# Kernel tuning notes

Measured on AMD Instinct MI355X. Metric: run time of the kernel, lower is better.

The kernel has to match this reference:

```python
import jax, jax.numpy as jnp
import numpy as np

N_NODES = 100000
N_EDGES = 1600000


def setup_inputs() -> dict:
    key = jax.random.key(0)
    k1, k2, k3, k4, k5, k6 = jax.random.split(key, 6)
    x = jax.random.normal(k1, (N_NODES, 2), dtype=jnp.float32)
    edge_index = jax.random.randint(k2, (2, N_EDGES), 0, N_NODES, dtype=jnp.int64)
    # Glorot-style init for GCN weights, zeros for biases (PyG defaults)
    W1 = jax.random.normal(k3, (2, 64), dtype=jnp.float32) * (1.0 / np.sqrt(2.0))
    b1 = jnp.zeros((64,), dtype=jnp.float32)
    W2 = jax.random.normal(k4, (64, 1), dtype=jnp.float32) * (1.0 / np.sqrt(64.0))
    b2 = jnp.zeros((1,), dtype=jnp.float32)
    return {"x": x, "edge_index": edge_index, "W1": W1, "b1": b1, "W2": W2, "b2": b2}


def reference(x, edge_index, W1, b1, W2, b2):
    N = x.shape[0]
    row, col = edge_index[0], edge_index[1]  # source, target (PyG flow source_to_target)
    # symmetric GCN normalization, degrees from target index (no self loops)
    deg = jax.ops.segment_sum(jnp.ones(edge_index.shape[1], x.dtype), col, num_segments=N)
    deg_inv_sqrt = jnp.where(deg > 0, jnp.where(deg > 0, deg, 1.0) ** -0.5, 0.0)
    norm = (deg_inv_sqrt[row] * deg_inv_sqrt[col])[:, None]  # [E,1]

    def gcn_conv(h, W, b):
        h = h @ W                       # [N,F_out] tiny GEMM
        msg = h[row] * norm             # gather + scale: [E,F_out]
        agg = jax.ops.segment_sum(msg, col, num_segments=N)  # scatter-add
        return agg + b

    h = jax.nn.relu(gcn_conv(x, W1, b1))   # dropout is identity in eval mode
    out = jax.nn.relu(gcn_conv(h, W2, b2))
    return out
```

## Files before the change

kernel.cpp:

```cpp
#include <hip/hip_runtime.h>
#include <math.h>

#define NN 100000
#define NE 1600000
#define BKT 448
#define NB 224
#define EPB 6400
#define NPB 250
#define STRIDE 8192
#define RT 1024

__global__ void __launch_bounds__(RT) reorder_kernel(
        const int* __restrict__ row, const int* __restrict__ col,
        unsigned* __restrict__ cursor, unsigned* __restrict__ packed) {
    __shared__ int h[NB], lb[NB];
    __shared__ unsigned gaddr[NB], glim[NB];
    __shared__ int wsum[RT / 64];
    __shared__ uint2 sga[EPB];
    const int t = threadIdx.x;
    const int lane = t & 63, wid = t >> 6;
    const int e0 = blockIdx.x * EPB;

    for (int i = t; i < NB; i += RT) h[i] = 0;
    __syncthreads();

    const int4* rv = (const int4*)(row + e0);
    const int4* cv = (const int4*)(col + e0);
    unsigned pk[8]; int bb[8];
#pragma unroll
    for (int u = 0; u < 8; ++u) bb[u] = -1;
#pragma unroll
    for (int g = 0; g < 2; ++g) {
        int grp = g * RT + t;
        if (grp < EPB / 4) {
            int4 r4 = rv[grp], c4 = cv[grp];
            int rr[4] = {r4.x, r4.y, r4.z, r4.w};
            int cc[4] = {c4.x, c4.y, c4.z, c4.w};
#pragma unroll
            for (int j = 0; j < 4; ++j) {
                int b = cc[j] / BKT;
                int cl = cc[j] - b * BKT;
                pk[4 * g + j] = ((unsigned)rr[j] << 9) | (unsigned)cl;
                bb[4 * g + j] = b;
            }
        }
    }
#pragma unroll
    for (int u = 0; u < 8; ++u)
        if (bb[u] >= 0) atomicAdd(&h[bb[u]], 1);
    __syncthreads();

    int v = (t < NB) ? h[t] : 0;
    int incl = v;
#pragma unroll
    for (int d = 1; d < 64; d <<= 1) {
        int u2 = __shfl_up(incl, d);
        if (lane >= d) incl += u2;
    }
    if (lane == 63) wsum[wid] = incl;
    __syncthreads();
    int off = 0;
#pragma unroll
    for (int j = 0; j < 3; ++j)
        if (j < wid) off += wsum[j];
    if (t < NB) {
        lb[t] = off + incl - v;
        unsigned base = v ? atomicAdd(&cursor[t], (unsigned)v) : 0u;
        gaddr[t] = (unsigned)t * STRIDE + base;
        glim[t]  = (unsigned)(t + 1) * STRIDE;
    }
    __syncthreads();
    for (int i = t; i < NB; i += RT) h[i] = 0;
    __syncthreads();

#pragma unroll
    for (int u = 0; u < 8; ++u) {
        if (bb[u] >= 0) {
            int b = bb[u];
            int r = atomicAdd(&h[b], 1);
            unsigned a = gaddr[b] + (unsigned)r;
            if (a >= glim[b]) a = 0xFFFFFFFFu;
            sga[lb[b] + r] = make_uint2(pk[u], a);
        }
    }
    __syncthreads();
    for (int i = t; i < EPB; i += RT) {
        uint2 e = sga[i];
        if (e.y != 0xFFFFFFFFu) packed[e.y] = e.x;
    }
}

__global__ void __launch_bounds__(RT) sortb_kernel(
        const unsigned* __restrict__ packed, const unsigned* __restrict__ cursor,
        const float2* __restrict__ x2,
        unsigned* __restrict__ srow, int2* __restrict__ node_rng,
        float* __restrict__ dis, float2* __restrict__ y2) {
    __shared__ int cnt[BKT], rk[BKT], sexA[BKT];
    __shared__ int wsum[(BKT + 63) / 64];
    __shared__ unsigned srt[STRIDE];
    const int t = threadIdx.x;
    const int lane = t & 63, wid = t >> 6;
    const int b = blockIdx.x;
    const unsigned s0 = (unsigned)b * STRIDE;
    const int L = min((int)cursor[b], STRIDE);
    const int L4 = L >> 2;

    for (int i = t; i < BKT; i += RT) { cnt[i] = 0; rk[i] = 0; }
    __syncthreads();

    const uint4* pv4 = (const uint4*)(packed + s0);
    for (int g = t; g < L4; g += RT) {
        uint4 p4 = pv4[g];
        atomicAdd(&cnt[p4.x & 511u], 1);
        atomicAdd(&cnt[p4.y & 511u], 1);
        atomicAdd(&cnt[p4.z & 511u], 1);
        atomicAdd(&cnt[p4.w & 511u], 1);
    }
    for (int i = 4 * L4 + t; i < L; i += RT)
        atomicAdd(&cnt[packed[s0 + i] & 511u], 1);
    __syncthreads();

    int v = (t < BKT) ? cnt[t] : 0;
    int incl = v;
#pragma unroll
    for (int d = 1; d < 64; d <<= 1) {
        int u2 = __shfl_up(incl, d);
        if (lane >= d) incl += u2;
    }
    if (lane == 63 && wid < (BKT + 63) / 64) wsum[wid] = incl;
    __syncthreads();
    int off = 0;
#pragma unroll
    for (int j = 0; j < (BKT + 63) / 64 - 1; ++j)
        if (j < wid) off += wsum[j];
    if (t < BKT) {
        int sex = off + incl - v;
        sexA[t] = sex;
        int node = b * BKT + t;
        if (node < NN) {
            float dv = (v > 0) ? rsqrtf((float)v) : 0.0f;
            dis[node] = dv;
            float2 xv = x2[node];
            y2[node] = make_float2(xv.x * dv, xv.y * dv);
            node_rng[node] = make_int2((int)(s0 + sex), (int)(s0 + sex + v));
        }
    }
    __syncthreads();

    for (int g = t; g < L4; g += RT) {
        uint4 p4 = pv4[g];
        unsigned pp[4] = {p4.x, p4.y, p4.z, p4.w};
#pragma unroll
        for (int j = 0; j < 4; ++j) {
            int cl = pp[j] & 511u;
            int r = atomicAdd(&rk[cl], 1);
            srt[sexA[cl] + r] = pp[j] >> 9;
        }
    }
    for (int i = 4 * L4 + t; i < L; i += RT) {
        unsigned p = packed[s0 + i];
        int cl = p & 511u;
        int r = atomicAdd(&rk[cl], 1);
        srt[sexA[cl] + r] = p >> 9;
    }
    __syncthreads();
    uint4* so4 = (uint4*)(srow + s0);
    for (int g = t; g < L4; g += RT) so4[g] = ((const uint4*)srt)[g];
    for (int i = 4 * L4 + t; i < L; i += RT) srow[s0 + i] = srt[i];
}

__global__ void conv1_kernel(const unsigned* __restrict__ srow, const int2* __restrict__ node_rng,
                             const float2* __restrict__ y2, const float* __restrict__ dis,
                             const float* __restrict__ W1, const float* __restrict__ b1,
                             const float* __restrict__ W2, float* __restrict__ z2) {
    __shared__ float sW0[64], sW1[64], sb1[64], sW2[64];
    int t = threadIdx.x;
    if (t < 64) { sW0[t] = W1[t]; sW1[t] = W1[64 + t]; sb1[t] = b1[t]; sW2[t] = W2[t]; }
    __syncthreads();
    int lane = t & 3;
    int node = blockIdx.x * 64 + (t >> 2);
    if (node >= NN) return;
    int2 rng = node_rng[node];
    float sx = 0.f, sy = 0.f;
    for (int k = rng.x + lane; k < rng.y; k += 4) {
        float2 v = y2[srow[k]];
        sx += v.x; sy += v.y;
    }
    sx += __shfl_xor(sx, 1); sy += __shfl_xor(sy, 1);
    sx += __shfl_xor(sx, 2); sy += __shfl_xor(sy, 2);
    float dv = dis[node];
    float a0 = sx * dv, a1 = sy * dv;
    float acc = 0.0f;
    int j0 = lane * 16;
#pragma unroll
    for (int jj = 0; jj < 16; ++jj) {
        int j = j0 + jj;
        float h = fmaf(a0, sW0[j], fmaf(a1, sW1[j], sb1[j]));
        acc = fmaf(fmaxf(h, 0.0f), sW2[j], acc);
    }
    acc += __shfl_xor(acc, 1);
    acc += __shfl_xor(acc, 2);
    if (lane == 0) z2[node] = acc * dv;
}

__global__ void conv2_kernel(const unsigned* __restrict__ srow, const int2* __restrict__ node_rng,
                             const float* __restrict__ z2, const float* __restrict__ dis,
                             const float* __restrict__ b2, float* __restrict__ out) {
    int t = threadIdx.x;
    int lane = t & 3;
    int node = blockIdx.x * 64 + (t >> 2);
    if (node >= NN) return;
    int2 rng = node_rng[node];
    float s = 0.f;
    for (int k = rng.x + lane; k < rng.y; k += 4)
        s += z2[srow[k]];
    s += __shfl_xor(s, 1);
    s += __shfl_xor(s, 2);
    if (lane == 0)
        out[node] = fmaxf(fmaf(dis[node], s, b2[0]), 0.0f);
}

extern "C" void kernel_launch(void* const* d_in, const int* in_sizes, int n_in,
                              void* d_out, int out_size, void* d_ws, size_t ws_size,
                              hipStream_t stream) {
    const float* x  = (const float*)d_in[0];
    const int*   ei = (const int*)d_in[1];
    const float* W1 = (const float*)d_in[2];
    const float* b1 = (const float*)d_in[3];
    const float* W2 = (const float*)d_in[4];
    const float* b2 = (const float*)d_in[5];
    float* out = (float*)d_out;

    const int* row = ei;
    const int* col = ei + NE;

    unsigned* packed   = (unsigned*)d_ws;
    unsigned* srow     = packed + (size_t)NB * STRIDE;
    float2*   y2       = (float2*)(srow + (size_t)NB * STRIDE);
    float*    dis      = (float*)(y2 + NN);
    float*    z2       = dis + NN;
    int2*     node_rng = (int2*)(z2 + NN);
    unsigned* cursor   = (unsigned*)(node_rng + NN);

    hipMemsetAsync(cursor, 0, NB * sizeof(unsigned), stream);

    reorder_kernel<<<NPB, RT, 0, stream>>>(row, col, cursor, packed);
    sortb_kernel  <<<NB, RT, 0, stream>>>(packed, cursor, (const float2*)x,
                                          srow, node_rng, dis, y2);
    conv1_kernel  <<<(NN + 63) / 64, 256, 0, stream>>>(srow, node_rng, y2, dis,
                                                       W1, b1, W2, z2);
    conv2_kernel  <<<(NN + 63) / 64, 256, 0, stream>>>(srow, node_rng, z2, dis, b2, out);
}
```

Measured before the change: 111.8 us.

## Split degree pass and fuse bucket sort with first GCN conv using LDS indices

Moves the degree/normalisation computation into its own kernel and fuses the per-bucket counting sort with the first convolution, so conv1 reads neighbour indices from shared memory instead of re-reading srow from global. Each node's segment is padded to a multiple of four, which enables uint4 index loads in both conv1 and conv2; STRIDE grows to make room for the padding. In exchange, the packed buffer is read one more time, conv1 now runs on only 224 blocks with fewer nodes processed in parallel, and the padding adds overflow clamping.

```diff
diff --git a/kernel.cpp b/kernel.cpp
--- a/kernel.cpp
+++ b/kernel.cpp
@@ -7,7 +7,7 @@
 #define NB 224
 #define EPB 6400
 #define NPB 250
-#define STRIDE 8192
+#define STRIDE 8960
 #define RT 1024
 
 __global__ void __launch_bounds__(RT) reorder_kernel(
@@ -90,22 +90,20 @@
     }
 }
 
-__global__ void __launch_bounds__(RT) sortb_kernel(
+__global__ void __launch_bounds__(RT) deg_kernel(
         const unsigned* __restrict__ packed, const unsigned* __restrict__ cursor,
-        const float2* __restrict__ x2,
-        unsigned* __restrict__ srow, int2* __restrict__ node_rng,
-        float* __restrict__ dis, float2* __restrict__ y2) {
-    __shared__ int cnt[BKT], rk[BKT], sexA[BKT];
-    __shared__ int wsum[(BKT + 63) / 64];
-    __shared__ unsigned srt[STRIDE];
+        const float2* __restrict__ x2, float* __restrict__ dis,
+        float2* __restrict__ y2, int2* __restrict__ node_rng) {
+    __shared__ int cnt[BKT];
+    __shared__ int wsum[7];
     const int t = threadIdx.x;
     const int lane = t & 63, wid = t >> 6;
     const int b = blockIdx.x;
-    const unsigned s0 = (unsigned)b * STRIDE;
+    const int s0 = b * STRIDE;
     const int L = min((int)cursor[b], STRIDE);
     const int L4 = L >> 2;
 
-    for (int i = t; i < BKT; i += RT) { cnt[i] = 0; rk[i] = 0; }
+    for (int i = t; i < BKT; i += RT) cnt[i] = 0;
     __syncthreads();
 
     const uint4* pv4 = (const uint4*)(packed + s0);
@@ -121,32 +119,66 @@
     __syncthreads();
 
     int v = (t < BKT) ? cnt[t] : 0;
-    int incl = v;
+    int vp = (v + 3) & ~3;
+    int incl = vp;
 #pragma unroll
     for (int d = 1; d < 64; d <<= 1) {
         int u2 = __shfl_up(incl, d);
         if (lane >= d) incl += u2;
     }
-    if (lane == 63 && wid < (BKT + 63) / 64) wsum[wid] = incl;
+    if (lane == 63 && wid < 7) wsum[wid] = incl;
     __syncthreads();
     int off = 0;
 #pragma unroll
-    for (int j = 0; j < (BKT + 63) / 64 - 1; ++j)
+    for (int j = 0; j < 6; ++j)
         if (j < wid) off += wsum[j];
     if (t < BKT) {
-        int sex = off + incl - v;
-        sexA[t] = sex;
+        int sex = off + incl - vp;
+        if (sex + v > STRIDE) v = max(0, STRIDE - sex);
         int node = b * BKT + t;
         if (node < NN) {
             float dv = (v > 0) ? rsqrtf((float)v) : 0.0f;
             dis[node] = dv;
             float2 xv = x2[node];
             y2[node] = make_float2(xv.x * dv, xv.y * dv);
-            node_rng[node] = make_int2((int)(s0 + sex), (int)(s0 + sex + v));
-        }
-    }
-    __syncthreads();
-
+            node_rng[node] = make_int2(s0 + sex, s0 + sex + v);
+        }
+    }
+}
+
+__global__ void __launch_bounds__(RT) sortcv1_kernel(
+        const unsigned* __restrict__ packed, const unsigned* __restrict__ cursor,
+        const int2* __restrict__ node_rng,
+        const float2* __restrict__ y2, const float* __restrict__ dis,
+        const float* __restrict__ W1, const float* __restrict__ b1,
+        const float* __restrict__ W2,
+        unsigned* __restrict__ srow, float* __restrict__ z2) {
+    __shared__ int sexA[BKT], vA[BKT], rk[BKT];
+    __shared__ unsigned srt[STRIDE];
+    __shared__ float sW0[64], sW1[64], sb1[64], sW2[64];
+    __shared__ int sLp;
+    const int t = threadIdx.x;
+    const int b = blockIdx.x;
+    const int s0 = b * STRIDE;
+    const int L = min((int)cursor[b], STRIDE);
+    const int L4 = L >> 2;
+
+    if (t < BKT) {
+        int node = b * BKT + t;
+        rk[t] = 0;
+        if (node < NN) {
+            int2 rng = node_rng[node];
+            sexA[t] = rng.x - s0;
+            vA[t] = rng.y - rng.x;
+        } else { sexA[t] = 0; vA[t] = 0; }
+    } else if (t < BKT + 64) {
+        int j = t - BKT;
+        sW0[j] = W1[j]; sW1[j] = W1[64 + j]; sb1[j] = b1[j]; sW2[j] = W2[j];
+    }
+    if (t == 0) sLp = 0;
+    __syncthreads();
+
+    const uint4* pv4 = (const uint4*)(packed + s0);
     for (int g = t; g < L4; g += RT) {
         uint4 p4 = pv4[g];
         unsigned pp[4] = {p4.x, p4.y, p4.z, p4.w};
@@ -154,53 +186,59 @@
         for (int j = 0; j < 4; ++j) {
             int cl = pp[j] & 511u;
             int r = atomicAdd(&rk[cl], 1);
-            srt[sexA[cl] + r] = pp[j] >> 9;
+            int idx = sexA[cl] + r;
+            if (idx < STRIDE) srt[idx] = pp[j] >> 9;
         }
     }
     for (int i = 4 * L4 + t; i < L; i += RT) {
         unsigned p = packed[s0 + i];
         int cl = p & 511u;
         int r = atomicAdd(&rk[cl], 1);
-        srt[sexA[cl] + r] = p >> 9;
-    }
-    __syncthreads();
+        int idx = sexA[cl] + r;
+        if (idx < STRIDE) srt[idx] = p >> 9;
+    }
+    if (t < BKT && vA[t] > 0) atomicMax(&sLp, sexA[t] + ((vA[t] + 3) & ~3));
+    __syncthreads();
+
+    const int Lp4 = sLp >> 2;
     uint4* so4 = (uint4*)(srow + s0);
-    for (int g = t; g < L4; g += RT) so4[g] = ((const uint4*)srt)[g];
-    for (int i = 4 * L4 + t; i < L; i += RT) srow[s0 + i] = srt[i];
-}
-
-__global__ void conv1_kernel(const unsigned* __restrict__ srow, const int2* __restrict__ node_rng,
-                             const float2* __restrict__ y2, const float* __restrict__ dis,
-                             const float* __restrict__ W1, const float* __restrict__ b1,
-                             const float* __restrict__ W2, float* __restrict__ z2) {
-    __shared__ float sW0[64], sW1[64], sb1[64], sW2[64];
-    int t = threadIdx.x;
-    if (t < 64) { sW0[t] = W1[t]; sW1[t] = W1[64 + t]; sb1[t] = b1[t]; sW2[t] = W2[t]; }
-    __syncthreads();
-    int lane = t & 3;
-    int node = blockIdx.x * 64 + (t >> 2);
-    if (node >= NN) return;
-    int2 rng = node_rng[node];
-    float sx = 0.f, sy = 0.f;
-    for (int k = rng.x + lane; k < rng.y; k += 4) {
-        float2 v = y2[srow[k]];
-        sx += v.x; sy += v.y;
-    }
-    sx += __shfl_xor(sx, 1); sy += __shfl_xor(sy, 1);
-    sx += __shfl_xor(sx, 2); sy += __shfl_xor(sy, 2);
-    float dv = dis[node];
-    float a0 = sx * dv, a1 = sy * dv;
-    float acc = 0.0f;
-    int j0 = lane * 16;
-#pragma unroll
-    for (int jj = 0; jj < 16; ++jj) {
-        int j = j0 + jj;
-        float h = fmaf(a0, sW0[j], fmaf(a1, sW1[j], sb1[j]));
-        acc = fmaf(fmaxf(h, 0.0f), sW2[j], acc);
-    }
-    acc += __shfl_xor(acc, 1);
-    acc += __shfl_xor(acc, 2);
-    if (lane == 0) z2[node] = acc * dv;
+    for (int g = t; g < Lp4; g += RT) so4[g] = ((const uint4*)srt)[g];
+
+    const int lane = t & 3;
+    const int q = t >> 2;
+    for (int nd = q; nd < BKT; nd += RT / 4) {
+        int node = b * BKT + nd;
+        if (node >= NN) break;
+        int v = vA[nd];
+        int base4 = sexA[nd] >> 2;
+        float sx = 0.f, sy = 0.f;
+        for (int g = lane; 4 * g < v; g += 4) {
+            uint4 i4 = ((const uint4*)srt)[base4 + g];
+            unsigned ii[4] = {i4.x, i4.y, i4.z, i4.w};
+#pragma unroll
+            for (int j = 0; j < 4; ++j) {
+                if (4 * g + j < v) {
+                    float2 vy = y2[ii[j]];
+                    sx += vy.x; sy += vy.y;
+                }
+            }
+        }
+        sx += __shfl_xor(sx, 1); sy += __shfl_xor(sy, 1);
+        sx += __shfl_xor(sx, 2); sy += __shfl_xor(sy, 2);
+        float dv = dis[node];
+        float a0 = sx * dv, a1 = sy * dv;
+        float acc = 0.0f;
+        const int j0 = lane * 16;
+#pragma unroll
+        for (int jj = 0; jj < 16; ++jj) {
+            int j = j0 + jj;
+            float h = fmaf(a0, sW0[j], fmaf(a1, sW1[j], sb1[j]));
+            acc = fmaf(fmaxf(h, 0.0f), sW2[j], acc);
+        }
+        acc += __shfl_xor(acc, 1);
+        acc += __shfl_xor(acc, 2);
+        if (lane == 0) z2[node] = acc * dv;
+    }
 }
 
 __global__ void conv2_kernel(const unsigned* __restrict__ srow, const int2* __restrict__ node_rng,
@@ -211,9 +249,16 @@
     int node = blockIdx.x * 64 + (t >> 2);
     if (node >= NN) return;
     int2 rng = node_rng[node];
+    int v = rng.y - rng.x;
+    const uint4* s4 = (const uint4*)(srow + rng.x);
     float s = 0.f;
-    for (int k = rng.x + lane; k < rng.y; k += 4)
-        s += z2[srow[k]];
+    for (int g = lane; 4 * g < v; g += 4) {
+        uint4 i4 = s4[g];
+        unsigned ii[4] = {i4.x, i4.y, i4.z, i4.w};
+#pragma unroll
+        for (int j = 0; j < 4; ++j)
+            if (4 * g + j < v) s += z2[ii[j]];
+    }
     s += __shfl_xor(s, 1);
     s += __shfl_xor(s, 2);
     if (lane == 0)
@@ -245,9 +290,9 @@
     hipMemsetAsync(cursor, 0, NB * sizeof(unsigned), stream);
 
     reorder_kernel<<<NPB, RT, 0, stream>>>(row, col, cursor, packed);
-    sortb_kernel  <<<NB, RT, 0, stream>>>(packed, cursor, (const float2*)x,
-                                          srow, node_rng, dis, y2);
-    conv1_kernel  <<<(NN + 63) / 64, 256, 0, stream>>>(srow, node_rng, y2, dis,
-                                                       W1, b1, W2, z2);
+    deg_kernel    <<<NB, RT, 0, stream>>>(packed, cursor, (const float2*)x,
+                                          dis, y2, node_rng);
+    sortcv1_kernel<<<NB, RT, 0, stream>>>(packed, cursor, node_rng, y2, dis,
+                                          W1, b1, W2, srow, z2);
     conv2_kernel  <<<(NN + 63) / 64, 256, 0, stream>>>(srow, node_rng, z2, dis, b2, out);
 }
```

Result: no change. 113.6 us (+1.6%).

## Pad per-node CSR segments to 16 bytes and use vector index loads in convs

Applied to the files above, without the earlier changes.

Each node's segment in the sorted neighbor array is padded to a multiple of four entries, and the bucket stride grows to make room. The conv kernels can then load neighbor indices as uint4 per lane instead of scalar loads, which cuts the number of index load instructions in the gather loops. In exchange it adds shared memory and global footprint, truncation guards for bucket overflow, and padding writes, and the per-lane work split changes so that low-degree nodes leave lanes idle.

```diff
diff --git a/kernel.cpp b/kernel.cpp
--- a/kernel.cpp
+++ b/kernel.cpp
@@ -7,7 +7,7 @@
 #define NB 224
 #define EPB 6400
 #define NPB 250
-#define STRIDE 8192
+#define STRIDE 9472
 #define RT 1024
 
 __global__ void __launch_bounds__(RT) reorder_kernel(
@@ -96,16 +96,18 @@
         unsigned* __restrict__ srow, int2* __restrict__ node_rng,
         float* __restrict__ dis, float2* __restrict__ y2) {
     __shared__ int cnt[BKT], rk[BKT], sexA[BKT];
-    __shared__ int wsum[(BKT + 63) / 64];
+    __shared__ int wsum[7];
     __shared__ unsigned srt[STRIDE];
+    __shared__ int sLp;
     const int t = threadIdx.x;
     const int lane = t & 63, wid = t >> 6;
     const int b = blockIdx.x;
-    const unsigned s0 = (unsigned)b * STRIDE;
+    const int s0 = b * STRIDE;
     const int L = min((int)cursor[b], STRIDE);
     const int L4 = L >> 2;
 
     for (int i = t; i < BKT; i += RT) { cnt[i] = 0; rk[i] = 0; }
+    if (t == 0) sLp = 0;
     __syncthreads();
 
     const uint4* pv4 = (const uint4*)(packed + s0);
@@ -121,28 +123,31 @@
     __syncthreads();
 
     int v = (t < BKT) ? cnt[t] : 0;
-    int incl = v;
+    int vp = (v + 3) & ~3;
+    int incl = vp;
 #pragma unroll
     for (int d = 1; d < 64; d <<= 1) {
         int u2 = __shfl_up(incl, d);
         if (lane >= d) incl += u2;
     }
-    if (lane == 63 && wid < (BKT + 63) / 64) wsum[wid] = incl;
+    if (lane == 63 && wid < 7) wsum[wid] = incl;
     __syncthreads();
     int off = 0;
 #pragma unroll
-    for (int j = 0; j < (BKT + 63) / 64 - 1; ++j)
+    for (int j = 0; j < 6; ++j)
         if (j < wid) off += wsum[j];
     if (t < BKT) {
-        int sex = off + incl - v;
+        int sex = off + incl - vp;
+        if (sex + v > STRIDE) v = max(0, STRIDE - sex);
         sexA[t] = sex;
+        if (v > 0) atomicMax(&sLp, sex + ((v + 3) & ~3));
         int node = b * BKT + t;
         if (node < NN) {
             float dv = (v > 0) ? rsqrtf((float)v) : 0.0f;
             dis[node] = dv;
             float2 xv = x2[node];
             y2[node] = make_float2(xv.x * dv, xv.y * dv);
-            node_rng[node] = make_int2((int)(s0 + sex), (int)(s0 + sex + v));
+            node_rng[node] = make_int2(s0 + sex, s0 + sex + v);
         }
     }
     __syncthreads();
@@ -154,19 +159,21 @@
         for (int j = 0; j < 4; ++j) {
             int cl = pp[j] & 511u;
             int r = atomicAdd(&rk[cl], 1);
-            srt[sexA[cl] + r] = pp[j] >> 9;
+            int idx = sexA[cl] + r;
+            if (idx < STRIDE) srt[idx] = pp[j] >> 9;
         }
     }
     for (int i = 4 * L4 + t; i < L; i += RT) {
         unsigned p = packed[s0 + i];
         int cl = p & 511u;
         int r = atomicAdd(&rk[cl], 1);
-        srt[sexA[cl] + r] = p >> 9;
-    }
-    __syncthreads();
+        int idx = sexA[cl] + r;
+        if (idx < STRIDE) srt[idx] = p >> 9;
+    }
+    __syncthreads();
+    const int Lp4 = sLp >> 2;
     uint4* so4 = (uint4*)(srow + s0);
-    for (int g = t; g < L4; g += RT) so4[g] = ((const uint4*)srt)[g];
-    for (int i = 4 * L4 + t; i < L; i += RT) srow[s0 + i] = srt[i];
+    for (int g = t; g < Lp4; g += RT) so4[g] = ((const uint4*)srt)[g];
 }
 
 __global__ void conv1_kernel(const unsigned* __restrict__ srow, const int2* __restrict__ node_rng,
@@ -181,10 +188,19 @@
     int node = blockIdx.x * 64 + (t >> 2);
     if (node >= NN) return;
     int2 rng = node_rng[node];
+    int v = rng.y - rng.x;
+    const uint4* s4 = (const uint4*)(srow + rng.x);
     float sx = 0.f, sy = 0.f;
-    for (int k = rng.x + lane; k < rng.y; k += 4) {
-        float2 v = y2[srow[k]];
-        sx += v.x; sy += v.y;
+    for (int g = lane; 4 * g < v; g += 4) {
+        uint4 i4 = s4[g];
+        unsigned ii[4] = {i4.x, i4.y, i4.z, i4.w};
+#pragma unroll
+        for (int j = 0; j < 4; ++j) {
+            if (4 * g + j < v) {
+                float2 vy = y2[ii[j]];
+                sx += vy.x; sy += vy.y;
+            }
+        }
     }
     sx += __shfl_xor(sx, 1); sy += __shfl_xor(sy, 1);
     sx += __shfl_xor(sx, 2); sy += __shfl_xor(sy, 2);
@@ -211,9 +227,16 @@
     int node = blockIdx.x * 64 + (t >> 2);
     if (node >= NN) return;
     int2 rng = node_rng[node];
+    int v = rng.y - rng.x;
+    const uint4* s4 = (const uint4*)(srow + rng.x);
     float s = 0.f;
-    for (int k = rng.x + lane; k < rng.y; k += 4)
-        s += z2[srow[k]];
+    for (int g = lane; 4 * g < v; g += 4) {
+        uint4 i4 = s4[g];
+        unsigned ii[4] = {i4.x, i4.y, i4.z, i4.w};
+#pragma unroll
+        for (int j = 0; j < 4; ++j)
+            if (4 * g + j < v) s += z2[ii[j]];
+    }
     s += __shfl_xor(s, 1);
     s += __shfl_xor(s, 2);
     if (lane == 0)
```

New measurement: 114.4 us. +2.3%, slower.
